# Optimization experiments

Hardware: AMD Instinct MI355X
Metric: run time of the kernel (lower is better)

## Reference

```python
import jax, jax.numpy as jnp
import numpy as np

N_NODES = 100000
N_EDGES = 1000000
D_IN = 64
D_MODEL = 64  # H * D
H = 4
D = D_MODEL // H


def setup_inputs() -> dict:
    key = jax.random.key(0)
    ks = jax.random.split(key, 9)
    nodes = jax.random.normal(ks[0], (N_NODES, D_IN), dtype=jnp.float32)
    senders = jax.random.randint(ks[1], (N_EDGES,), 0, N_NODES, dtype=jnp.int32)
    receivers = jnp.sort(jax.random.randint(ks[2], (N_EDGES,), 0, N_NODES, dtype=jnp.int32))
    s = 1.0 / np.sqrt(D_IN)
    W_qk = jax.random.uniform(ks[3], (D_IN, D_MODEL), jnp.float32, -s, s)
    b_qk = jnp.zeros((D_MODEL,), jnp.float32)
    W_v = jax.random.uniform(ks[4], (D_IN, D_MODEL), jnp.float32, -s, s)
    b_v = jnp.zeros((D_MODEL,), jnp.float32)
    so = 1.0 / np.sqrt(D_MODEL)
    W_out = jax.random.uniform(ks[5], (D_MODEL, D_MODEL), jnp.float32, -so, so)
    b_out = jnp.zeros((D_MODEL,), jnp.float32)
    return {
        'nodes': nodes, 'W_qk': W_qk, 'b_qk': b_qk, 'W_v': W_v, 'b_v': b_v,
        'W_out': W_out, 'b_out': b_out, 'senders': senders, 'receivers': receivers,
    }


def _segment_softmax(logits, segment_ids, num_segments):
    # jraph-style numerically stable segment softmax (segments are sorted)
    maxs = jax.ops.segment_max(logits, segment_ids, num_segments, indices_are_sorted=True)
    e = jnp.exp(logits - maxs[segment_ids])
    z = jax.ops.segment_sum(e, segment_ids, num_segments, indices_are_sorted=True)
    return e / z[segment_ids]


def reference(nodes, W_qk, b_qk, W_v, b_v, W_out, b_out, senders, receivers):
    N = nodes.shape[0]
    # projections: N (H D) -> N H D
    qks = (nodes @ W_qk + b_qk).reshape(N, H, D)
    vs = (nodes @ W_v + b_v).reshape(N, H, D)
    # per-edge QK scores: [E, H]
    scores = jnp.einsum('ehd,ehd->eh', qks[receivers], qks[senders])
    attn = _segment_softmax(scores, receivers, N)
    # weighted message scatter: [E,H,D] -> [N, H*D]
    messages = (attn[..., None] * vs[senders]).reshape(-1, H * D)
    ctx = jax.ops.segment_sum(messages, receivers, N, indices_are_sorted=True)
    out = ctx @ W_out + b_out
    return out, attn
```

## Files before the change

kernel.cpp:

```cpp
#include <hip/hip_runtime.h>
#include <math.h>


typedef _Float16 h2 __attribute__((ext_vector_type(2)));
typedef _Float16 half8 __attribute__((ext_vector_type(8)));
typedef float floatx4 __attribute__((ext_vector_type(4)));

#define SP_ROW 136
#define SW_ROW 72

__global__ __launch_bounds__(256) void mhga_proj(
    const float* __restrict__ X,
    const float* __restrict__ Wqk, const float* __restrict__ Wv,
    const float* __restrict__ bqk, const float* __restrict__ bv,
    unsigned char* __restrict__ packed,
    const int* __restrict__ receivers, int* __restrict__ row_ptr,
    int N, int E, int PB)
{
    if ((int)blockIdx.x >= PB) {
        const int n = (blockIdx.x - PB) * 256 + threadIdx.x;
        if (n > N) return;
        int lo = 0, hi = E;
        while (lo < hi) {
            const int mid = (lo + hi) >> 1;
            if (receivers[mid] < n) lo = mid + 1; else hi = mid;
        }
        row_ptr[n] = lo;
        return;
    }

    __shared__ __align__(16) _Float16 sP[64 * SP_ROW];
    __shared__ __align__(16) _Float16 sW[128 * SW_ROW];
    const int t = threadIdx.x;
    const int w = t >> 6, lane = t & 63;
    const int ln = lane & 15, quad = lane >> 4;
    const int m0 = blockIdx.x * 64;

    for (int i = t; i < 8192; i += 256) {
        const int hf = i >> 12;
        const int j = i & 4095;
        const int k = j >> 6, mp = j & 63;
        const float wv = hf ? Wv[j] : Wqk[j];
        sW[(hf * 64 + mp) * SW_ROW + k] = (_Float16)wv;
    }

    const int arow = min(m0 + w * 16 + ln, N - 1);
    const float* xr = X + (size_t)arow * 64;
    const float4 xa = *(const float4*)(xr + quad * 8);
    const float4 xb = *(const float4*)(xr + quad * 8 + 4);
    const float4 xc = *(const float4*)(xr + 32 + quad * 8);
    const float4 xd = *(const float4*)(xr + 32 + quad * 8 + 4);
    const half8 a0 = { (_Float16)xa.x, (_Float16)xa.y, (_Float16)xa.z,
                       (_Float16)xa.w, (_Float16)xb.x, (_Float16)xb.y,
                       (_Float16)xb.z, (_Float16)xb.w };
    const half8 a1 = { (_Float16)xc.x, (_Float16)xc.y, (_Float16)xc.z,
                       (_Float16)xc.w, (_Float16)xd.x, (_Float16)xd.y,
                       (_Float16)xd.z, (_Float16)xd.w };

    __syncthreads();

    floatx4 acc[8];
#pragma unroll
    for (int tt = 0; tt < 8; ++tt) {
        const _Float16* wrow = sW + (tt * 16 + ln) * SW_ROW;
        const half8 b0 = *(const half8*)(wrow + quad * 8);
        const half8 b1 = *(const half8*)(wrow + 32 + quad * 8);
        floatx4 c = {0.f, 0.f, 0.f, 0.f};
        c = __builtin_amdgcn_mfma_f32_16x16x32_f16(a0, b0, c, 0, 0, 0);
        c = __builtin_amdgcn_mfma_f32_16x16x32_f16(a1, b1, c, 0, 0, 0);
        acc[tt] = c;
    }

#pragma unroll
    for (int tt = 0; tt < 8; ++tt) {
        const float bt = (tt < 4) ? bqk[tt * 16 + ln] : bv[(tt - 4) * 16 + ln];
        const int j = (tt & 3) * 16 + ln;
        const int fidx = (j >> 2) * 8 + ((tt < 4) ? 0 : 4) + (j & 3);
#pragma unroll
        for (int r = 0; r < 4; ++r) {
            const int lrow = w * 16 + quad * 4 + r;
            sP[lrow * SP_ROW + fidx] = (_Float16)(acc[tt][r] + bt);
        }
    }

    const int crow = w * 16 + (lane >> 2);
    const int grow = m0 + crow;
    if (grow < N) {
        const _Float16* src = sP + crow * SP_ROW + (lane & 3) * 32;
        unsigned char* dst = packed + (size_t)grow * 256 + (lane & 3) * 64;
#pragma unroll
        for (int c = 0; c < 4; ++c)
            *(uint4*)(dst + c * 16) = *(const uint4*)(src + c * 8);
    }
}

__global__ __launch_bounds__(256) void mhga_attn(
    const unsigned char* __restrict__ packed,
    const int* __restrict__ senders, const int* __restrict__ row_ptr,
    const float* __restrict__ Wout, const float* __restrict__ bout,
    float* __restrict__ out, float* __restrict__ attn_out,
    int N, int NW)
{
    __shared__ float sAtt[4][256];
    __shared__ __align__(16) _Float16 sC[4][16][76];
    const int t = threadIdx.x;
    const int wave = t >> 6, lane = t & 63;
    const int g = lane >> 4, tl = lane & 15;

    const int W = blockIdx.x * 4 + wave;
    const int count = (W < N) ? ((N - W + NW - 1) / NW) : 0;

    for (int i = 0; i < count; ++i) {
        const int n = W + i * NW;
        const int e0 = row_ptr[n];
        const int e1 = row_ptr[n + 1];
        const int cnt = e1 - e0;

        float l = 0.f;
        float4 ctx = make_float4(0.f, 0.f, 0.f, 0.f);
        const uint2 qpk = *(const uint2*)(packed + (size_t)n * 256 + tl * 16);
        const h2 q0 = __builtin_bit_cast(h2, qpk.x);
        const h2 q1 = __builtin_bit_cast(h2, qpk.y);

        if (cnt <= 64) {
            int sid = 0;
            if (e0 + lane < e1) sid = senders[e0 + lane];
            const int iters = (cnt + 3) >> 2;
            const int s0 = __shfl(sid, g, 64);
            uint4 pk = *(const uint4*)(packed + (size_t)s0 * 256 + tl * 16);
            for (int it = 0; it < iters; ++it) {
                uint4 pkn = pk;
                if (it + 1 < iters) {
                    const int sn = __shfl(sid, (it + 1) * 4 + g, 64);
                    pkn = *(const uint4*)(packed + (size_t)sn * 256 + tl * 16);
                }
                const int idx = it * 4 + g;
                const h2 k0 = __builtin_bit_cast(h2, pk.x);
                const h2 k1 = __builtin_bit_cast(h2, pk.y);
                const h2 v0 = __builtin_bit_cast(h2, pk.z);
                const h2 v1 = __builtin_bit_cast(h2, pk.w);
                float d = __builtin_amdgcn_fdot2(q0, k0, 0.f, false);
                d = __builtin_amdgcn_fdot2(q1, k1, d, false);
                d += __shfl_xor(d, 1, 64);
                d += __shfl_xor(d, 2, 64);
                float p = __expf(d);
                p = (idx < cnt) ? p : 0.f;
                if ((tl & 3) == 0)
                    sAtt[wave][idx * 4 + (tl >> 2)] = p;
                l += p;
                ctx.x = fmaf(p, (float)v0.x, ctx.x);
                ctx.y = fmaf(p, (float)v0.y, ctx.y);
                ctx.z = fmaf(p, (float)v1.x, ctx.z);
                ctx.w = fmaf(p, (float)v1.y, ctx.w);
                pk = pkn;
            }
        } else {
            for (int base = e0; base < e1; base += 64) {
                const int c2 = min(64, e1 - base);
                int sid2 = 0;
                if (base + lane < e1) sid2 = senders[base + lane];
                const int it2 = (c2 + 3) >> 2;
                for (int ii = 0; ii < it2; ++ii) {
                    const int idx = ii * 4 + g;
                    const int s = __shfl(sid2, idx, 64);
                    if (idx < c2) {
                        const uint4 pk =
                            *(const uint4*)(packed + (size_t)s * 256 + tl * 16);
                        const h2 k0 = __builtin_bit_cast(h2, pk.x);
                        const h2 k1 = __builtin_bit_cast(h2, pk.y);
                        const h2 v0 = __builtin_bit_cast(h2, pk.z);
                        const h2 v1 = __builtin_bit_cast(h2, pk.w);
                        float d = __builtin_amdgcn_fdot2(q0, k0, 0.f, false);
                        d = __builtin_amdgcn_fdot2(q1, k1, d, false);
                        d += __shfl_xor(d, 1, 64);
                        d += __shfl_xor(d, 2, 64);
                        const float p = __expf(d);
                        if ((tl & 3) == 0)
                            attn_out[(size_t)(base + idx) * 4 + (tl >> 2)] = p;
                        l += p;
                        ctx.x = fmaf(p, (float)v0.x, ctx.x);
                        ctx.y = fmaf(p, (float)v0.y, ctx.y);
                        ctx.z = fmaf(p, (float)v1.x, ctx.z);
                        ctx.w = fmaf(p, (float)v1.y, ctx.w);
                    }
                }
            }
        }

#pragma unroll
        for (int mask = 16; mask <= 32; mask <<= 1) {
            l     += __shfl_xor(l, mask, 64);
            ctx.x += __shfl_xor(ctx.x, mask, 64);
            ctx.y += __shfl_xor(ctx.y, mask, 64);
            ctx.z += __shfl_xor(ctx.z, mask, 64);
            ctx.w += __shfl_xor(ctx.w, mask, 64);
        }
        const float inv = (l > 0.f) ? (1.f / l) : 0.f;

        const float lh = __shfl(l, (lane & 3) << 2, 64);
        const float invl = (lh > 0.f) ? (1.f / lh) : 0.f;
        if (cnt <= 64) {
            const int cnt4 = cnt * 4;
            for (int f = lane; f < cnt4; f += 64)
                attn_out[e0 * 4 + f] = sAtt[wave][f] * invl;
        } else {
            __builtin_amdgcn_s_waitcnt(0x0F70);
            volatile const float* vp = attn_out;
            for (int f = e0 * 4 + lane; f < e1 * 4; f += 64)
                attn_out[f] = vp[f] * invl;
        }

        if (g == 0) {
            const h2 c01 = { (_Float16)(ctx.x * inv), (_Float16)(ctx.y * inv) };
            const h2 c23 = { (_Float16)(ctx.z * inv), (_Float16)(ctx.w * inv) };
            uint2 pc;
            pc.x = __builtin_bit_cast(unsigned int, c01);
            pc.y = __builtin_bit_cast(unsigned int, c23);
            *(uint2*)(&sC[wave][i][tl * 4]) = pc;
        }
    }

    const half8 a0 = *(const half8*)(&sC[wave][tl][g * 8]);
    const half8 a1 = *(const half8*)(&sC[wave][tl][32 + g * 8]);
#pragma unroll
    for (int tt = 0; tt < 4; ++tt) {
        half8 b0, b1;
#pragma unroll
        for (int j = 0; j < 8; ++j) {
            b0[j] = (_Float16)Wout[(g * 8 + j) * 64 + tt * 16 + tl];
            b1[j] = (_Float16)Wout[(32 + g * 8 + j) * 64 + tt * 16 + tl];
        }
        floatx4 c = {0.f, 0.f, 0.f, 0.f};
        c = __builtin_amdgcn_mfma_f32_16x16x32_f16(a0, b0, c, 0, 0, 0);
        c = __builtin_amdgcn_mfma_f32_16x16x32_f16(a1, b1, c, 0, 0, 0);
        const float bt = bout[tt * 16 + tl];
#pragma unroll
        for (int r = 0; r < 4; ++r) {
            const int lrow = g * 4 + r;
            if (lrow < count)
                out[(size_t)(W + (size_t)lrow * NW) * 64 + tt * 16 + tl] =
                    c[r] + bt;
        }
    }
}

extern "C" void kernel_launch(void* const* d_in, const int* in_sizes, int n_in,
                              void* d_out, int out_size, void* d_ws, size_t ws_size,
                              hipStream_t stream) {
    const float* nodes   = (const float*)d_in[0];
    const float* W_qk    = (const float*)d_in[1];
    const float* b_qk    = (const float*)d_in[2];
    const float* W_v     = (const float*)d_in[3];
    const float* b_v     = (const float*)d_in[4];
    const float* W_out   = (const float*)d_in[5];
    const float* b_out   = (const float*)d_in[6];
    const int* senders   = (const int*)d_in[7];
    const int* receivers = (const int*)d_in[8];

    const int N = in_sizes[0] / 64;
    const int E = in_sizes[7];

    float* out      = (float*)d_out;
    float* attn_out = out + (size_t)N * 64;

    unsigned char* packed = (unsigned char*)d_ws;
    int* rowp = (int*)(packed + (size_t)N * 256);

    const int PB = (N + 63) / 64;
    const int RB = (N + 1 + 255) / 256;
    mhga_proj<<<PB + RB, 256, 0, stream>>>(nodes, W_qk, W_v, b_qk, b_v,
                                           packed, receivers, rowp, N, E, PB);
    const int NW = 2048 * 4;
    mhga_attn<<<2048, 256, 0, stream>>>(packed, senders, rowp, W_out, b_out,
                                        out, attn_out, N, NW);
}
```

Before: 179.9 us.

## Balance attention work per wave by edge-weighted contiguous node ranges

Replaces the strided node-to-wave assignment with contiguous node ranges chosen by binary search over row_ptr, weighted by edges plus a per-node constant, so each wave gets a similar amount of work. Contiguous ranges also let consecutive row_ptr values be reused and make the output writes and the gathers of query and sender rows more local. The output projection now runs per chunk of 16 nodes inside the loop. The cost is two binary searches per wave at kernel start and possible imbalance where degree varies strongly.

```diff
diff --git a/kernel.cpp b/kernel.cpp
--- a/kernel.cpp
+++ b/kernel.cpp
@@ -99,7 +99,7 @@
     const int* __restrict__ senders, const int* __restrict__ row_ptr,
     const float* __restrict__ Wout, const float* __restrict__ bout,
     float* __restrict__ out, float* __restrict__ attn_out,
-    int N, int NW)
+    int N, int E, int NW)
 {
     __shared__ float sAtt[4][256];
     __shared__ __align__(16) _Float16 sC[4][16][76];
@@ -108,138 +108,167 @@
     const int g = lane >> 4, tl = lane & 15;
 
     const int W = blockIdx.x * 4 + wave;
-    const int count = (W < N) ? ((N - W + NW - 1) / NW) : 0;
-
-    for (int i = 0; i < count; ++i) {
-        const int n = W + i * NW;
-        const int e0 = row_ptr[n];
-        const int e1 = row_ptr[n + 1];
-        const int cnt = e1 - e0;
-
-        float l = 0.f;
-        float4 ctx = make_float4(0.f, 0.f, 0.f, 0.f);
-        const uint2 qpk = *(const uint2*)(packed + (size_t)n * 256 + tl * 16);
-        const h2 q0 = __builtin_bit_cast(h2, qpk.x);
-        const h2 q1 = __builtin_bit_cast(h2, qpk.y);
-
-        if (cnt <= 64) {
-            int sid = 0;
-            if (e0 + lane < e1) sid = senders[e0 + lane];
-            const int iters = (cnt + 3) >> 2;
-            const int s0 = __shfl(sid, g, 64);
-            uint4 pk = *(const uint4*)(packed + (size_t)s0 * 256 + tl * 16);
-            for (int it = 0; it < iters; ++it) {
-                uint4 pkn = pk;
-                if (it + 1 < iters) {
-                    const int sn = __shfl(sid, (it + 1) * 4 + g, 64);
-                    pkn = *(const uint4*)(packed + (size_t)sn * 256 + tl * 16);
+
+    const long long Ctot = (long long)E + 8LL * N;
+    long long tgt0 = ((long long)W * Ctot) / NW;
+    long long tgt1 = ((long long)(W + 1) * Ctot) / NW;
+    int n0, n1;
+    {
+        int lo = 0, hi = N;
+        while (lo < hi) {
+            const int mid = (lo + hi) >> 1;
+            if ((long long)row_ptr[mid] + 8LL * mid < tgt0) lo = mid + 1;
+            else hi = mid;
+        }
+        n0 = lo;
+        hi = N;
+        while (lo < hi) {
+            const int mid = (lo + hi) >> 1;
+            if ((long long)row_ptr[mid] + 8LL * mid < tgt1) lo = mid + 1;
+            else hi = mid;
+        }
+        n1 = (W + 1 == NW) ? N : lo;
+    }
+
+    int e_run = (n0 < n1) ? row_ptr[n0] : 0;
+
+    for (int ns = n0; ns < n1; ns += 16) {
+        const int cc = min(16, n1 - ns);
+        for (int i = 0; i < cc; ++i) {
+            const int n = ns + i;
+            const int e0 = e_run;
+            const int e1 = row_ptr[n + 1];
+            e_run = e1;
+            const int cnt = e1 - e0;
+
+            float l = 0.f;
+            float4 ctx = make_float4(0.f, 0.f, 0.f, 0.f);
+            const uint2 qpk =
+                *(const uint2*)(packed + (size_t)n * 256 + tl * 16);
+            const h2 q0 = __builtin_bit_cast(h2, qpk.x);
+            const h2 q1 = __builtin_bit_cast(h2, qpk.y);
+
+            if (cnt <= 64) {
+                int sid = 0;
+                if (e0 + lane < e1) sid = senders[e0 + lane];
+                const int iters = (cnt + 3) >> 2;
+                const int s0 = __shfl(sid, g, 64);
+                uint4 pk = *(const uint4*)(packed + (size_t)s0 * 256 + tl * 16);
+                for (int it = 0; it < iters; ++it) {
+                    uint4 pkn = pk;
+                    if (it + 1 < iters) {
+                        const int sn = __shfl(sid, (it + 1) * 4 + g, 64);
+                        pkn = *(const uint4*)(packed +
+                                              (size_t)sn * 256 + tl * 16);
+                    }
+                    const int idx = it * 4 + g;
+                    const h2 k0 = __builtin_bit_cast(h2, pk.x);
+                    const h2 k1 = __builtin_bit_cast(h2, pk.y);
+                    const h2 v0 = __builtin_bit_cast(h2, pk.z);
+                    const h2 v1 = __builtin_bit_cast(h2, pk.w);
+                    float d = __builtin_amdgcn_fdot2(q0, k0, 0.f, false);
+                    d = __builtin_amdgcn_fdot2(q1, k1, d, false);
+                    d += __shfl_xor(d, 1, 64);
+                    d += __shfl_xor(d, 2, 64);
+                    float p = __expf(d);
+                    p = (idx < cnt) ? p : 0.f;
+                    if ((tl & 3) == 0)
+                        sAtt[wave][idx * 4 + (tl >> 2)] = p;
+                    l += p;
+                    ctx.x = fmaf(p, (float)v0.x, ctx.x);
+                    ctx.y = fmaf(p, (float)v0.y, ctx.y);
+                    ctx.z = fmaf(p, (float)v1.x, ctx.z);
+                    ctx.w = fmaf(p, (float)v1.y, ctx.w);
+                    pk = pkn;
                 }
-                const int idx = it * 4 + g;
-                const h2 k0 = __builtin_bit_cast(h2, pk.x);
-                const h2 k1 = __builtin_bit_cast(h2, pk.y);
-                const h2 v0 = __builtin_bit_cast(h2, pk.z);
-                const h2 v1 = __builtin_bit_cast(h2, pk.w);
-                float d = __builtin_amdgcn_fdot2(q0, k0, 0.f, false);
-                d = __builtin_amdgcn_fdot2(q1, k1, d, false);
-                d += __shfl_xor(d, 1, 64);
-                d += __shfl_xor(d, 2, 64);
-                float p = __expf(d);
-                p = (idx < cnt) ? p : 0.f;
-                if ((tl & 3) == 0)
-                    sAtt[wave][idx * 4 + (tl >> 2)] = p;
-                l += p;
-                ctx.x = fmaf(p, (float)v0.x, ctx.x);
-                ctx.y = fmaf(p, (float)v0.y, ctx.y);
-                ctx.z = fmaf(p, (float)v1.x, ctx.z);
-                ctx.w = fmaf(p, (float)v1.y, ctx.w);
-                pk = pkn;
-            }
-        } else {
-            for (int base = e0; base < e1; base += 64) {
-                const int c2 = min(64, e1 - base);
-                int sid2 = 0;
-                if (base + lane < e1) sid2 = senders[base + lane];
-                const int it2 = (c2 + 3) >> 2;
-                for (int ii = 0; ii < it2; ++ii) {
-                    const int idx = ii * 4 + g;
-                    const int s = __shfl(sid2, idx, 64);
-                    if (idx < c2) {
-                        const uint4 pk =
-                            *(const uint4*)(packed + (size_t)s * 256 + tl * 16);
-                        const h2 k0 = __builtin_bit_cast(h2, pk.x);
-                        const h2 k1 = __builtin_bit_cast(h2, pk.y);
-                        const h2 v0 = __builtin_bit_cast(h2, pk.z);
-                        const h2 v1 = __builtin_bit_cast(h2, pk.w);
-                        float d = __builtin_amdgcn_fdot2(q0, k0, 0.f, false);
-                        d = __builtin_amdgcn_fdot2(q1, k1, d, false);
-                        d += __shfl_xor(d, 1, 64);
-                        d += __shfl_xor(d, 2, 64);
-                        const float p = __expf(d);
-                        if ((tl & 3) == 0)
-                            attn_out[(size_t)(base + idx) * 4 + (tl >> 2)] = p;
-                        l += p;
-                        ctx.x = fmaf(p, (float)v0.x, ctx.x);
-                        ctx.y = fmaf(p, (float)v0.y, ctx.y);
-                        ctx.z = fmaf(p, (float)v1.x, ctx.z);
-                        ctx.w = fmaf(p, (float)v1.y, ctx.w);
+            } else {
+                for (int base = e0; base < e1; base += 64) {
+                    const int c2 = min(64, e1 - base);
+                    int sid2 = 0;
+                    if (base + lane < e1) sid2 = senders[base + lane];
+                    const int it2 = (c2 + 3) >> 2;
+                    for (int ii = 0; ii < it2; ++ii) {
+                        const int idx = ii * 4 + g;
+                        const int s = __shfl(sid2, idx, 64);
+                        if (idx < c2) {
+                            const uint4 pk = *(const uint4*)(
+                                packed + (size_t)s * 256 + tl * 16);
+                            const h2 k0 = __builtin_bit_cast(h2, pk.x);
+                            const h2 k1 = __builtin_bit_cast(h2, pk.y);
+                            const h2 v0 = __builtin_bit_cast(h2, pk.z);
+                            const h2 v1 = __builtin_bit_cast(h2, pk.w);
+                            float d = __builtin_amdgcn_fdot2(q0, k0, 0.f, false);
+                            d = __builtin_amdgcn_fdot2(q1, k1, d, false);
+                            d += __shfl_xor(d, 1, 64);
+                            d += __shfl_xor(d, 2, 64);
+                            const float p = __expf(d);
+                            if ((tl & 3) == 0)
+                                attn_out[(size_t)(base + idx) * 4 + (tl >> 2)] = p;
+                            l += p;
+                            ctx.x = fmaf(p, (float)v0.x, ctx.x);
+                            ctx.y = fmaf(p, (float)v0.y, ctx.y);
+                            ctx.z = fmaf(p, (float)v1.x, ctx.z);
+                            ctx.w = fmaf(p, (float)v1.y, ctx.w);
+                        }
                     }
                 }
             }
-        }
-
-#pragma unroll
-        for (int mask = 16; mask <= 32; mask <<= 1) {
-            l     += __shfl_xor(l, mask, 64);
-            ctx.x += __shfl_xor(ctx.x, mask, 64);
-            ctx.y += __shfl_xor(ctx.y, mask, 64);
-            ctx.z += __shfl_xor(ctx.z, mask, 64);
-            ctx.w += __shfl_xor(ctx.w, mask, 64);
-        }
-        const float inv = (l > 0.f) ? (1.f / l) : 0.f;
-
-        const float lh = __shfl(l, (lane & 3) << 2, 64);
-        const float invl = (lh > 0.f) ? (1.f / lh) : 0.f;
-        if (cnt <= 64) {
-            const int cnt4 = cnt * 4;
-            for (int f = lane; f < cnt4; f += 64)
-                attn_out[e0 * 4 + f] = sAtt[wave][f] * invl;
-        } else {
-            __builtin_amdgcn_s_waitcnt(0x0F70);
-            volatile const float* vp = attn_out;
-            for (int f = e0 * 4 + lane; f < e1 * 4; f += 64)
-                attn_out[f] = vp[f] * invl;
-        }
-
-        if (g == 0) {
-            const h2 c01 = { (_Float16)(ctx.x * inv), (_Float16)(ctx.y * inv) };
-            const h2 c23 = { (_Float16)(ctx.z * inv), (_Float16)(ctx.w * inv) };
-            uint2 pc;
-            pc.x = __builtin_bit_cast(unsigned int, c01);
-            pc.y = __builtin_bit_cast(unsigned int, c23);
-            *(uint2*)(&sC[wave][i][tl * 4]) = pc;
-        }
-    }
-
-    const half8 a0 = *(const half8*)(&sC[wave][tl][g * 8]);
-    const half8 a1 = *(const half8*)(&sC[wave][tl][32 + g * 8]);
-#pragma unroll
-    for (int tt = 0; tt < 4; ++tt) {
-        half8 b0, b1;
-#pragma unroll
-        for (int j = 0; j < 8; ++j) {
-            b0[j] = (_Float16)Wout[(g * 8 + j) * 64 + tt * 16 + tl];
-            b1[j] = (_Float16)Wout[(32 + g * 8 + j) * 64 + tt * 16 + tl];
-        }
-        floatx4 c = {0.f, 0.f, 0.f, 0.f};
-        c = __builtin_amdgcn_mfma_f32_16x16x32_f16(a0, b0, c, 0, 0, 0);
-        c = __builtin_amdgcn_mfma_f32_16x16x32_f16(a1, b1, c, 0, 0, 0);
-        const float bt = bout[tt * 16 + tl];
-#pragma unroll
-        for (int r = 0; r < 4; ++r) {
-            const int lrow = g * 4 + r;
-            if (lrow < count)
-                out[(size_t)(W + (size_t)lrow * NW) * 64 + tt * 16 + tl] =
-                    c[r] + bt;
+
+#pragma unroll
+            for (int mask = 16; mask <= 32; mask <<= 1) {
+                l     += __shfl_xor(l, mask, 64);
+                ctx.x += __shfl_xor(ctx.x, mask, 64);
+                ctx.y += __shfl_xor(ctx.y, mask, 64);
+                ctx.z += __shfl_xor(ctx.z, mask, 64);
+                ctx.w += __shfl_xor(ctx.w, mask, 64);
+            }
+            const float inv = (l > 0.f) ? (1.f / l) : 0.f;
+
+            const float lh = __shfl(l, (lane & 3) << 2, 64);
+            const float invl = (lh > 0.f) ? (1.f / lh) : 0.f;
+            if (cnt <= 64) {
+                const int cnt4 = cnt * 4;
+                for (int f = lane; f < cnt4; f += 64)
+                    attn_out[e0 * 4 + f] = sAtt[wave][f] * invl;
+            } else {
+                __builtin_amdgcn_s_waitcnt(0x0F70);
+                volatile const float* vp = attn_out;
+                for (int f = e0 * 4 + lane; f < e1 * 4; f += 64)
+                    attn_out[f] = vp[f] * invl;
+            }
+
+            if (g == 0) {
+                const h2 c01 = { (_Float16)(ctx.x * inv),
+                                 (_Float16)(ctx.y * inv) };
+                const h2 c23 = { (_Float16)(ctx.z * inv),
+                                 (_Float16)(ctx.w * inv) };
+                uint2 pc;
+                pc.x = __builtin_bit_cast(unsigned int, c01);
+                pc.y = __builtin_bit_cast(unsigned int, c23);
+                *(uint2*)(&sC[wave][i][tl * 4]) = pc;
+            }
+        }
+
+        const half8 a0 = *(const half8*)(&sC[wave][tl][g * 8]);
+        const half8 a1 = *(const half8*)(&sC[wave][tl][32 + g * 8]);
+#pragma unroll
+        for (int tt = 0; tt < 4; ++tt) {
+            half8 b0, b1;
+#pragma unroll
+            for (int j = 0; j < 8; ++j) {
+                b0[j] = (_Float16)Wout[(g * 8 + j) * 64 + tt * 16 + tl];
+                b1[j] = (_Float16)Wout[(32 + g * 8 + j) * 64 + tt * 16 + tl];
+            }
+            floatx4 c = {0.f, 0.f, 0.f, 0.f};
+            c = __builtin_amdgcn_mfma_f32_16x16x32_f16(a0, b0, c, 0, 0, 0);
+            c = __builtin_amdgcn_mfma_f32_16x16x32_f16(a1, b1, c, 0, 0, 0);
+            const float bt = bout[tt * 16 + tl];
+#pragma unroll
+            for (int r = 0; r < 4; ++r) {
+                const int lrow = g * 4 + r;
+                if (lrow < cc)
+                    out[(size_t)(ns + lrow) * 64 + tt * 16 + tl] = c[r] + bt;
+            }
         }
     }
 }
@@ -272,5 +301,5 @@
                                            packed, receivers, rowp, N, E, PB);
     const int NW = 2048 * 4;
     mhga_attn<<<2048, 256, 0, stream>>>(packed, senders, rowp, W_out, b_out,
-                                        out, attn_out, N, NW);
+                                        out, attn_out, N, E, NW);
 }
```

New measurement: 195.7 us. 1.09x slower.
